# Performance work log

Hardware: AMD Instinct MI355X
Metric: run time of the kernel (lower is better)

## Reference

```python
import jax, jax.numpy as jnp
import numpy as np

B, T, C, H = 2, 2048, 1024, 16
Dh = C // H  # 64
EPS = 1e-5


def layer_norm(x, g, b):
    mu = jnp.mean(x, axis=-1, keepdims=True)
    var = jnp.mean(jnp.square(x - mu), axis=-1, keepdims=True)
    return (x - mu) * jax.lax.rsqrt(var + EPS) * g + b


def setup_inputs() -> dict:
    key = jax.random.key(0)
    ks = jax.random.split(key, 12)
    s = 0.02
    return {
        "x": jax.random.normal(ks[0], (B, T, C), dtype=jnp.float32),
        # per-head projections, stacked: (H, C, Dh), no bias (bias=False in source)
        "Wq": jax.random.normal(ks[1], (H, C, Dh), dtype=jnp.float32) * s,
        "Wk": jax.random.normal(ks[2], (H, C, Dh), dtype=jnp.float32) * s,
        "Wv": jax.random.normal(ks[3], (H, C, Dh), dtype=jnp.float32) * s,
        "Wo": jax.random.normal(ks[4], (H * Dh, C), dtype=jnp.float32) * s,
        "bo": jnp.zeros((C,), dtype=jnp.float32),
        "W1": jax.random.normal(ks[5], (C, 4 * C), dtype=jnp.float32) * s,
        "b1": jnp.zeros((4 * C,), dtype=jnp.float32),
        "W2": jax.random.normal(ks[6], (4 * C, C), dtype=jnp.float32) * s,
        "b2": jnp.zeros((C,), dtype=jnp.float32),
        "g1": jnp.ones((C,), dtype=jnp.float32),
        "be1": jnp.zeros((C,), dtype=jnp.float32),
        "g2": jnp.ones((C,), dtype=jnp.float32),
        "be2": jnp.zeros((C,), dtype=jnp.float32),
    }


def reference(x, Wq, Wk, Wv, Wo, bo, W1, b1, W2, b2, g1, be1, g2, be2):
    # --- self-attention sublayer ---
    h = layer_norm(x, g1, be1)                       # (B,T,C)
    q = jnp.einsum("btc,hcd->bhtd", h, Wq)
    k = jnp.einsum("btc,hcd->bhtd", h, Wk)
    v = jnp.einsum("btc,hcd->bhtd", h, Wv)
    # NOTE: source scales by C**-0.5 (head INPUT dim), not head_size**-0.5
    scores = jnp.einsum("bhqd,bhkd->bhqk", q, k) * (C ** -0.5)
    # encoder=True default => mask is all ones => no masking applied
    w = jax.nn.softmax(scores, axis=-1)              # (B,H,T,T)
    o = jnp.einsum("bhqk,bhkd->bhqd", w, v)          # (B,H,T,Dh)
    o = o.transpose(0, 2, 1, 3).reshape(B, T, H * Dh)  # concat heads
    attn = o @ Wo + bo                               # output projection
    x = x + attn
    # --- feed-forward sublayer ---
    h2 = layer_norm(x, g2, be2)
    ff = jax.nn.relu(h2 @ W1 + b1) @ W2 + b2
    return x + ff
```

## Files before the change

kernel.cpp:

```cpp
#include <hip/hip_runtime.h>
#include <hip/hip_bf16.h>

#define BT   4096
#define CD   1024
#define TD   2048
#define NH   16
#define DH   64
#define BB   2

typedef __attribute__((ext_vector_type(8))) short bf16x8;
typedef __attribute__((ext_vector_type(4))) short bf16x4;
typedef __attribute__((ext_vector_type(4))) float f32x4;
typedef __attribute__((ext_vector_type(2))) unsigned int u32x2;
typedef __attribute__((ext_vector_type(4))) unsigned int u32x4;

__device__ inline short f2bf(float f) {
    union { float fv; unsigned u; } x; x.fv = f;
    unsigned r = x.u + 0x7fffu + ((x.u >> 16) & 1u);
    return (short)(r >> 16);
}
__device__ inline float bf2f(short s) {
    union { unsigned u; float f; } x; x.u = ((unsigned)(unsigned short)s) << 16;
    return x.f;
}
__device__ inline unsigned pk2bf(float a, float b) {
    union { __hip_bfloat162 h; unsigned u; } cv;
    cv.h = __float22bfloat162_rn(float2{a, b});
    return cv.u;
}

#if __has_builtin(__builtin_amdgcn_exp2f)
#define EXP2(x) __builtin_amdgcn_exp2f(x)
#else
#define EXP2(x) exp2f(x)
#endif

__device__ inline void gload_lds16(const short* g, short* lds) {
    __builtin_amdgcn_global_load_lds(
        (const __attribute__((address_space(1))) void*)g,
        (__attribute__((address_space(3))) void*)lds, 16, 0, 0);
}

__launch_bounds__(256)
__global__ void ln_kernel(const float* __restrict__ x,
                          const float* __restrict__ g,
                          const float* __restrict__ be,
                          short* __restrict__ out) {
    __shared__ float red[2][4];
    const int row = blockIdx.x;
    const float* xr = x + (size_t)row * CD;
    float s = 0.f, ss = 0.f;
    for (int c = threadIdx.x; c < CD; c += 256) {
        float v = xr[c];
        s += v; ss += v * v;
    }
    #pragma unroll
    for (int off = 32; off > 0; off >>= 1) {
        s  += __shfl_down(s,  off, 64);
        ss += __shfl_down(ss, off, 64);
    }
    int wid = threadIdx.x >> 6, lane = threadIdx.x & 63;
    if (lane == 0) { red[0][wid] = s; red[1][wid] = ss; }
    __syncthreads();
    float sum   = red[0][0] + red[0][1] + red[0][2] + red[0][3];
    float sumsq = red[1][0] + red[1][1] + red[1][2] + red[1][3];
    float mu   = sum * (1.f / CD);
    float var  = sumsq * (1.f / CD) - mu * mu;
    float rstd = rsqrtf(var + 1e-5f);
    short* orow = out + (size_t)row * CD;
    for (int c = threadIdx.x; c < CD; c += 256) {
        float v = xr[c];
        orow[c] = f2bf((v - mu) * rstd * g[c] + be[c]);
    }
}

__launch_bounds__(256)
__global__ void prep_weights(const float* __restrict__ Wq, const float* __restrict__ Wk,
                             const float* __restrict__ Wv, const float* __restrict__ Wo,
                             const float* __restrict__ W1, const float* __restrict__ W2,
                             short* __restrict__ wqt, short* __restrict__ wot,
                             short* __restrict__ w1t, short* __restrict__ w2t) {
    __shared__ float tt[64][65];
    const int id = blockIdx.x;
    const float* in; short* out; int R, Cc, r0, c0;
    if (id < 768) {
        int which = id >> 8, rem = id & 255, hh = rem >> 4, ry = rem & 15;
        in  = (which == 0 ? Wq : which == 1 ? Wk : Wv) + (size_t)hh * CD * DH;
        out = wqt + (size_t)which * CD * CD + (size_t)hh * DH * CD;
        R = CD; Cc = DH; r0 = ry * 64; c0 = 0;
    } else if (id < 1024) {
        int t = id - 768;  in = Wo; out = wot; R = CD;     Cc = CD;     r0 = (t >> 4) * 64; c0 = (t & 15) * 64;
    } else if (id < 2048) {
        int t = id - 1024; in = W1; out = w1t; R = CD;     Cc = 4 * CD; r0 = (t >> 6) * 64; c0 = (t & 63) * 64;
    } else {
        int t = id - 2048; in = W2; out = w2t; R = 4 * CD; Cc = CD;     r0 = (t >> 4) * 64; c0 = (t & 15) * 64;
    }
    const int tid = threadIdx.x;
    #pragma unroll
    for (int i = 0; i < 16; ++i) {
        int e = i * 256 + tid;
        tt[e >> 6][e & 63] = in[(size_t)(r0 + (e >> 6)) * Cc + c0 + (e & 63)];
    }
    __syncthreads();
    #pragma unroll
    for (int i = 0; i < 16; ++i) {
        int e = i * 256 + tid;
        out[(size_t)(c0 + (e >> 6)) * R + r0 + (e & 63)] = f2bf(tt[e & 63][e >> 6]);
    }
}

__launch_bounds__(256)
__global__ void vtrans(const short* __restrict__ vin, short* __restrict__ vout) {
    __shared__ short t[64 * 65];
    const int tid = threadIdx.x;
    const int bh = blockIdx.y;
    const int t0 = blockIdx.x * 64;
    const int b = bh >> 4, h = bh & 15;
    const short* src = vin + (size_t)b * TD * CD + (size_t)h * DH;
    short* dst = vout + (size_t)bh * DH * TD;
    #pragma unroll
    for (int i = 0; i < 16; ++i) {
        int e = i * 256 + tid;
        t[(e >> 6) * 65 + (e & 63)] = src[(size_t)(t0 + (e >> 6)) * CD + (e & 63)];
    }
    __syncthreads();
    #pragma unroll
    for (int i = 0; i < 16; ++i) {
        int e = i * 256 + tid;
        int d = e >> 6, tt = e & 63;
        dst[(size_t)d * TD + t0 + tt] = t[tt * 65 + d];
    }
}

template <int MODE, int TN, int GR>
__launch_bounds__(GR * 256)
__global__ void gemm_mfma(const short* __restrict__ A,
                          const short* __restrict__ Bt,
                          const float* __restrict__ bias,
                          const float* __restrict__ resid,
                          float* __restrict__ outf,
                          short* __restrict__ outb,
                          int N, int K) {
    __shared__ __align__(16) short smem[GR * 3 * (128 + TN) * 32];
    const int tid = threadIdx.x;
    const int kgrp = (GR == 2) ? (tid >> 8) : 0;
    const int tid256 = tid & 255;
    const int w4 = tid256 >> 6, lane = tid & 63;
    const int quad = lane >> 4, l16 = lane & 15;
    const int wr = w4 >> 1, wc = w4 & 1;
    const int li = blockIdx.y * gridDim.x + blockIdx.x;
    const int m0 = ((li & 7) * 4 + ((li >> 3) & 3)) * 128;
    const int n0 = (li >> 5) * TN;
    const int NT = TN / 32;
    const int kbase = kgrp * (K / GR);

    short* grpBase = smem + (size_t)kgrp * 3 * (128 + TN) * 32;
#define AS(bi) (grpBase + (bi) * (128 + TN) * 32)
#define BS(bi) (AS(bi) + 128 * 32)

    f32x4 acc[4][NT] = {};

    auto STAGE = [&](int kt, int bi) {
        const int k0 = kbase + kt * 32;
        short* as = AS(bi);
        short* bs = BS(bi);
        #pragma unroll
        for (int i = 0; i < 2; ++i) {
            int s = i * 256 + tid256;
            int row = s >> 2, kc = (s & 3) ^ ((row >> 1) & 3);
            gload_lds16(A + (size_t)(m0 + row) * K + k0 + kc * 8,
                        &as[(i * 256 + w4 * 64) * 8]);
        }
        #pragma unroll
        for (int i = 0; i < TN / 64; ++i) {
            int s = i * 256 + tid256;
            int row = s >> 2, kc = (s & 3) ^ ((row >> 1) & 3);
            gload_lds16(Bt + (size_t)(n0 + row) * K + k0 + kc * 8,
                        &bs[(i * 256 + w4 * 64) * 8]);
        }
    };

    auto COMPUTE = [&](int bi) {
        const int xo = (quad ^ ((l16 >> 1) & 3)) * 8;
        const short* as = AS(bi);
        const short* bs = BS(bi);
        bf16x8 a[4], b[NT];
        #pragma unroll
        for (int mt = 0; mt < 4; ++mt)
            a[mt] = *(const bf16x8*)&as[(wr * 64 + mt * 16 + l16) * 32 + xo];
        #pragma unroll
        for (int nt = 0; nt < NT; ++nt)
            b[nt] = *(const bf16x8*)&bs[(wc * (TN / 2) + nt * 16 + l16) * 32 + xo];
        #pragma unroll
        for (int mt = 0; mt < 4; ++mt)
            #pragma unroll
            for (int nt = 0; nt < NT; ++nt)
                acc[mt][nt] = __builtin_amdgcn_mfma_f32_16x16x32_bf16(a[mt], b[nt], acc[mt][nt], 0, 0, 0);
    };

    const int nk = (K / GR) >> 5;
    STAGE(0, 0);
    STAGE(1, 1);
    int bi = 0;
    for (int t = 0; t < nk - 1; ++t) {
        asm volatile("s_waitcnt vmcnt(4)" ::: "memory");
        __builtin_amdgcn_s_barrier();
        asm volatile("" ::: "memory");
        int bn = bi + 2 >= 3 ? bi - 1 : bi + 2;
        if (t + 2 < nk) STAGE(t + 2, bn);
        COMPUTE(bi);
        bi = bi + 1 >= 3 ? 0 : bi + 1;
    }
    asm volatile("s_waitcnt vmcnt(0)" ::: "memory");
    __builtin_amdgcn_s_barrier();
    asm volatile("" ::: "memory");
    COMPUTE(bi);

    if (GR == 2) {
        float* red = (float*)smem;
        __syncthreads();
        if (kgrp == 1) {
            #pragma unroll
            for (int mt = 0; mt < 4; ++mt)
                #pragma unroll
                for (int nt = 0; nt < NT; ++nt)
                    *(f32x4*)&red[((mt * NT + nt) * 256 + w4 * 64 + lane) * 4] = acc[mt][nt];
        }
        __syncthreads();
        if (kgrp == 1) return;
        #pragma unroll
        for (int mt = 0; mt < 4; ++mt)
            #pragma unroll
            for (int nt = 0; nt < NT; ++nt) {
                f32x4 p = *(const f32x4*)&red[((mt * NT + nt) * 256 + w4 * 64 + lane) * 4];
                acc[mt][nt] += p;
            }
    }

    const float qsc = (MODE == 5 && n0 < CD) ? 0.03125f * 1.44269504f : 1.0f;
    short* ob5 = (MODE == 5) ? outb + (size_t)(n0 >> 10) * BT * CD : nullptr;

    #pragma unroll
    for (int mt = 0; mt < 4; ++mt)
        #pragma unroll
        for (int nt = 0; nt < NT; ++nt)
            #pragma unroll
            for (int reg = 0; reg < 4; ++reg) {
                int row = m0 + wr * 64 + mt * 16 + quad * 4 + reg;
                int col = n0 + wc * (TN / 2) + nt * 16 + l16;
                float v = acc[mt][nt][reg];
                if (MODE == 1) { v += bias[col] + resid[(size_t)row * N + col];
                                 outf[(size_t)row * N + col] = v; }
                if (MODE == 2) { v = fmaxf(v + bias[col], 0.f);
                                 outb[(size_t)row * N + col] = f2bf(v); }
                if (MODE == 5) { ob5[(size_t)row * CD + (col & 1023)] = f2bf(v * qsc); }
            }
#undef AS
#undef BS
}

#define BQ   128
#define BK   64
#define STR  68

__launch_bounds__(256)
__global__ void attn_mfma(const short* __restrict__ q,
                          const short* __restrict__ k,
                          const short* __restrict__ vt,
                          short* __restrict__ opart,
                          float* __restrict__ lpart) {
    __shared__ short Ks[2][BK * STR];
    __shared__ short Vt[2][DH * STR];

    const int tid  = threadIdx.x;
    const int w = tid >> 6, lane = tid & 63;
    const int quad = lane >> 4, l16 = lane & 15;
    const int h = blockIdx.y;
    const int b = blockIdx.z >> 1, split = blockIdx.z & 1;
    const int q0 = blockIdx.x * BQ;
    const size_t base  = (size_t)b * TD * CD + (size_t)h * DH;
    const size_t vbase = (size_t)(b * NH + h) * DH * TD;

    bf16x8 qf[2][2];
    #pragma unroll
    for (int rt = 0; rt < 2; ++rt) {
        const short* qp = q + base + (size_t)(q0 + w * 32 + rt * 16 + l16) * CD;
        qf[rt][0] = *(const bf16x8*)&qp[quad * 8];
        qf[rt][1] = *(const bf16x8*)&qp[32 + quad * 8];
    }

    float l_p[2] = {};
    f32x4 O[2][4] = {};

    const int kbeg = split * (TD / 2);
    const int NTI = (TD / 2) / BK;

    const int r8 = tid >> 3, c8 = (tid & 7) * 8;
    const int s32 = ((r8 & 4) << 2) + ((r8 >> 3) << 2) + (r8 & 3);
    const short* kg = k + base + c8;
    const short* vg = vt + vbase + (size_t)r8 * TD + c8;

#define ISSUE_T(t, K0, K1, V0, V1) do {                                   \
        const size_t ko_ = (size_t)(kbeg + (t) * BK);                     \
        K0 = *(const bf16x8*)&kg[(ko_ + r8) * CD];                        \
        K1 = *(const bf16x8*)&kg[(ko_ + r8 + 32) * CD];                   \
        V0 = *(const bf16x8*)&vg[ko_];                                    \
        V1 = *(const bf16x8*)&vg[(size_t)32 * TD + ko_];                  \
    } while (0)

#define WRITE_T(buf, K0, K1, V0, V1) do {                                 \
        *(bf16x8*)&Ks[buf][s32 * STR + c8] = K0;                          \
        *(bf16x8*)&Ks[buf][(s32 + 32) * STR + c8] = K1;                   \
        *(bf16x8*)&Vt[buf][r8 * STR + c8] = V0;                           \
        *(bf16x8*)&Vt[buf][(r8 + 32) * STR + c8] = V1;                    \
    } while (0)

#define COMPUTE_T(buf) do {                                               \
        __builtin_amdgcn_s_setprio(1);                                    \
        _Pragma("unroll")                                                 \
        for (int sp = 0; sp < 2; ++sp) {                                  \
            bf16x8 kbe0 = *(const bf16x8*)&Ks[buf][(sp * 32 + l16) * STR + quad * 8];      \
            bf16x8 kbe1 = *(const bf16x8*)&Ks[buf][(sp * 32 + l16) * STR + 32 + quad * 8]; \
            bf16x8 kbo0 = *(const bf16x8*)&Ks[buf][(sp * 32 + 16 + l16) * STR + quad * 8]; \
            bf16x8 kbo1 = *(const bf16x8*)&Ks[buf][(sp * 32 + 16 + l16) * STR + 32 + quad * 8]; \
            bf16x8 pa8[2];                                                \
            _Pragma("unroll")                                             \
            for (int rt = 0; rt < 2; ++rt) {                              \
                f32x4 ae = (f32x4){0.f, 0.f, 0.f, 0.f};                   \
                f32x4 ao = (f32x4){0.f, 0.f, 0.f, 0.f};                   \
                ae = __builtin_amdgcn_mfma_f32_16x16x32_bf16(kbe0, qf[rt][0], ae, 0, 0, 0); \
                ae = __builtin_amdgcn_mfma_f32_16x16x32_bf16(kbe1, qf[rt][1], ae, 0, 0, 0); \
                ao = __builtin_amdgcn_mfma_f32_16x16x32_bf16(kbo0, qf[rt][0], ao, 0, 0, 0); \
                ao = __builtin_amdgcn_mfma_f32_16x16x32_bf16(kbo1, qf[rt][1], ao, 0, 0, 0); \
                float pe0 = EXP2(ae[0]), pe1 = EXP2(ae[1]);               \
                float pe2 = EXP2(ae[2]), pe3 = EXP2(ae[3]);               \
                float po0 = EXP2(ao[0]), po1 = EXP2(ao[1]);               \
                float po2 = EXP2(ao[2]), po3 = EXP2(ao[3]);               \
                l_p[rt] += ((pe0 + pe1) + (pe2 + pe3)) + ((po0 + po1) + (po2 + po3)); \
                union { u32x4 u; bf16x8 s; } cv_;                         \
                cv_.u = (u32x4){pk2bf(pe0, pe1), pk2bf(pe2, pe3),         \
                                pk2bf(po0, po1), pk2bf(po2, po3)};        \
                pa8[rt] = cv_.s;                                          \
            }                                                             \
            _Pragma("unroll")                                             \
            for (int dt = 0; dt < 4; ++dt) {                              \
                bf16x8 vb = *(const bf16x8*)&Vt[buf][(dt * 16 + l16) * STR + sp * 32 + quad * 8]; \
                O[0][dt] = __builtin_amdgcn_mfma_f32_16x16x32_bf16(pa8[0], vb, O[0][dt], 0, 0, 0); \
                O[1][dt] = __builtin_amdgcn_mfma_f32_16x16x32_bf16(pa8[1], vb, O[1][dt], 0, 0, 0); \
            }                                                             \
        }                                                                 \
        __builtin_amdgcn_s_setprio(0);                                    \
    } while (0)

    bf16x8 kA0, kA1, vA0, vA1;
    bf16x8 kB0, kB1, vB0, vB1;

    ISSUE_T(0, kA0, kA1, vA0, vA1);
    WRITE_T(0, kA0, kA1, vA0, vA1);
    ISSUE_T(1, kA0, kA1, vA0, vA1);
    __syncthreads();

    for (int it = 0; it < NTI; it += 2) {
        if (it + 2 < NTI) ISSUE_T(it + 2, kB0, kB1, vB0, vB1);
        COMPUTE_T(0);
        WRITE_T(1, kA0, kA1, vA0, vA1);
        __syncthreads();
        if (it + 3 < NTI) ISSUE_T(it + 3, kA0, kA1, vA0, vA1);
        COMPUTE_T(1);
        if (it + 2 < NTI) WRITE_T(0, kB0, kB1, vB0, vB1);
        __syncthreads();
    }
#undef ISSUE_T
#undef WRITE_T
#undef COMPUTE_T

    short* osp = opart + (size_t)split * BT * CD;
    float* lsp = lpart + (size_t)split * BB * NH * TD + (size_t)(b * NH + h) * TD;
    #pragma unroll
    for (int rt = 0; rt < 2; ++rt) {
        float l = l_p[rt];
        l += __shfl_xor(l, 16, 64);
        l += __shfl_xor(l, 32, 64);
        if (lane < 16) lsp[q0 + w * 32 + rt * 16 + lane] = l;
        #pragma unroll
        for (int reg = 0; reg < 4; ++reg) {
            int row = q0 + w * 32 + rt * 16 + quad * 4 + reg;
            short* op = osp + base + (size_t)row * CD;
            #pragma unroll
            for (int dt = 0; dt < 4; ++dt)
                op[dt * 16 + l16] = f2bf(O[rt][dt][reg]);
        }
    }
}

__launch_bounds__(256)
__global__ void attn_combine(const short* __restrict__ opart,
                             const float* __restrict__ lpart,
                             short* __restrict__ ob) {
    const size_t idx = ((size_t)blockIdx.x * 256 + threadIdx.x) * 8;
    const int row = (int)(idx >> 10);
    const int col = (int)(idx & 1023);
    const int b = row >> 11, qq = row & (TD - 1), hh = col >> 6;
    const size_t lbase = (size_t)(b * NH + hh) * TD + qq;
    const float l0 = lpart[lbase];
    const float l1 = lpart[(size_t)BB * NH * TD + lbase];
    const float inv = 1.f / (l0 + l1);
    bf16x8 a = *(const bf16x8*)&opart[idx];
    bf16x8 c = *(const bf16x8*)&opart[(size_t)BT * CD + idx];
    bf16x8 r;
    #pragma unroll
    for (int j = 0; j < 8; ++j)
        r[j] = f2bf((bf2f(a[j]) + bf2f(c[j])) * inv);
    *(bf16x8*)&ob[idx] = r;
}

extern "C" void kernel_launch(void* const* d_in, const int* in_sizes, int n_in,
                              void* d_out, int out_size, void* d_ws, size_t ws_size,
                              hipStream_t stream) {
    const float* x   = (const float*)d_in[0];
    const float* Wq  = (const float*)d_in[1];
    const float* Wk  = (const float*)d_in[2];
    const float* Wv  = (const float*)d_in[3];
    const float* Wo  = (const float*)d_in[4];
    const float* bo  = (const float*)d_in[5];
    const float* W1  = (const float*)d_in[6];
    const float* b1  = (const float*)d_in[7];
    const float* W2  = (const float*)d_in[8];
    const float* b2  = (const float*)d_in[9];
    const float* g1  = (const float*)d_in[10];
    const float* be1 = (const float*)d_in[11];
    const float* g2  = (const float*)d_in[12];
    const float* be2 = (const float*)d_in[13];
    float* out = (float*)d_out;

    const size_t SZ = (size_t)BT * CD;
    float* ws  = (float*)d_ws;
    short* qbf = (short*)ws;
    short* kbf = qbf + SZ;
    short* vbf = qbf + 2 * SZ;
    float* lpart = ws + SZ + SZ / 2;
    short* opart = (short*)(ws + 2 * SZ);
    float* x1  = ws + 2 * SZ;
    short* h   = (short*)(ws + 3 * SZ);
    short* ob  = (short*)(ws + 3 * SZ + SZ / 2);
    short* wqt = (short*)(ws + 4 * SZ);
    short* wot = wqt + 3 * CD * CD;
    short* w1t = (short*)(ws + 4 * SZ + SZ / 2);
    short* w2t = (short*)(ws + 5 * SZ);
    short* vtg = (short*)(ws + 5 * SZ + SZ / 2);
    short* ff1 = (short*)ws;

    ln_kernel<<<BT, 256, 0, stream>>>(x, g1, be1, h);

    prep_weights<<<3072, 256, 0, stream>>>(Wq, Wk, Wv, Wo, W1, W2, wqt, wot, w1t, w2t);

    gemm_mfma<5, 128, 1><<<dim3(24, 32), 256, 0, stream>>>(h, wqt, nullptr, nullptr, nullptr, qbf, 3 * CD, CD);

    vtrans<<<dim3(TD / 64, 2 * NH), 256, 0, stream>>>(vbf, vtg);

    attn_mfma<<<dim3(TD / BQ, NH, BB * 2), 256, 0, stream>>>(qbf, kbf, vtg, opart, lpart);

    attn_combine<<<dim3((int)(SZ / (256 * 8))), 256, 0, stream>>>(opart, lpart, ob);

    gemm_mfma<1, 128, 2><<<dim3(8, 32), 512, 0, stream>>>(ob, wot, bo, x, x1, nullptr, CD, CD);

    ln_kernel<<<BT, 256, 0, stream>>>(x1, g2, be2, h);

    gemm_mfma<2, 128, 1><<<dim3(32, 32), 256, 0, stream>>>(h, w1t, b1, nullptr, nullptr, ff1, 4 * CD, CD);

    gemm_mfma<1, 128, 2><<<dim3(8, 32), 512, 0, stream>>>(ff1, w2t, b2, x1, out, nullptr, CD, 4 * CD);
}
```

Baseline: 324.0 us.

## Compute softmax row sums via MFMA with ones and vectorize LN/prep loads

```diff
diff --git a/kernel.cpp b/kernel.cpp
--- a/kernel.cpp
+++ b/kernel.cpp
@@ -48,12 +48,11 @@
                           short* __restrict__ out) {
     __shared__ float red[2][4];
     const int row = blockIdx.x;
+    const int c4 = threadIdx.x * 4;
     const float* xr = x + (size_t)row * CD;
-    float s = 0.f, ss = 0.f;
-    for (int c = threadIdx.x; c < CD; c += 256) {
-        float v = xr[c];
-        s += v; ss += v * v;
-    }
+    float4 v = *(const float4*)&xr[c4];
+    float s  = (v.x + v.y) + (v.z + v.w);
+    float ss = (v.x * v.x + v.y * v.y) + (v.z * v.z + v.w * v.w);
     #pragma unroll
     for (int off = 32; off > 0; off >>= 1) {
         s  += __shfl_down(s,  off, 64);
@@ -67,11 +66,14 @@
     float mu   = sum * (1.f / CD);
     float var  = sumsq * (1.f / CD) - mu * mu;
     float rstd = rsqrtf(var + 1e-5f);
-    short* orow = out + (size_t)row * CD;
-    for (int c = threadIdx.x; c < CD; c += 256) {
-        float v = xr[c];
-        orow[c] = f2bf((v - mu) * rstd * g[c] + be[c]);
-    }
+    float4 gv = *(const float4*)&g[c4];
+    float4 bv = *(const float4*)&be[c4];
+    bf16x4 o;
+    o[0] = f2bf((v.x - mu) * rstd * gv.x + bv.x);
+    o[1] = f2bf((v.y - mu) * rstd * gv.y + bv.y);
+    o[2] = f2bf((v.z - mu) * rstd * gv.z + bv.z);
+    o[3] = f2bf((v.w - mu) * rstd * gv.w + bv.w);
+    *(bf16x4*)&out[(size_t)row * CD + c4] = o;
 }
 
 __launch_bounds__(256)
@@ -97,9 +99,14 @@
     }
     const int tid = threadIdx.x;
     #pragma unroll
-    for (int i = 0; i < 16; ++i) {
-        int e = i * 256 + tid;
-        tt[e >> 6][e & 63] = in[(size_t)(r0 + (e >> 6)) * Cc + c0 + (e & 63)];
+    for (int i = 0; i < 4; ++i) {
+        int f = i * 256 + tid;
+        int r = f >> 4, cc = (f & 15) * 4;
+        float4 vv = *(const float4*)&in[(size_t)(r0 + r) * Cc + c0 + cc];
+        tt[r][cc]     = vv.x;
+        tt[r][cc + 1] = vv.y;
+        tt[r][cc + 2] = vv.z;
+        tt[r][cc + 3] = vv.w;
     }
     __syncthreads();
     #pragma unroll
@@ -289,7 +296,9 @@
         qf[rt][1] = *(const bf16x8*)&qp[32 + quad * 8];
     }
 
-    float l_p[2] = {};
+    const bf16x8 ones = {(short)0x3F80, (short)0x3F80, (short)0x3F80, (short)0x3F80,
+                         (short)0x3F80, (short)0x3F80, (short)0x3F80, (short)0x3F80};
+    f32x4 O_l[2] = {};
     f32x4 O[2][4] = {};
 
     const int kbeg = split * (TD / 2);
@@ -336,7 +345,6 @@
                 float pe2 = EXP2(ae[2]), pe3 = EXP2(ae[3]);               \
                 float po0 = EXP2(ao[0]), po1 = EXP2(ao[1]);               \
                 float po2 = EXP2(ao[2]), po3 = EXP2(ao[3]);               \
-                l_p[rt] += ((pe0 + pe1) + (pe2 + pe3)) + ((po0 + po1) + (po2 + po3)); \
                 union { u32x4 u; bf16x8 s; } cv_;                         \
                 cv_.u = (u32x4){pk2bf(pe0, pe1), pk2bf(pe2, pe3),         \
                                 pk2bf(po0, po1), pk2bf(po2, po3)};        \
@@ -348,6 +356,8 @@
                 O[0][dt] = __builtin_amdgcn_mfma_f32_16x16x32_bf16(pa8[0], vb, O[0][dt], 0, 0, 0); \
                 O[1][dt] = __builtin_amdgcn_mfma_f32_16x16x32_bf16(pa8[1], vb, O[1][dt], 0, 0, 0); \
             }                                                             \
+            O_l[0] = __builtin_amdgcn_mfma_f32_16x16x32_bf16(pa8[0], ones, O_l[0], 0, 0, 0); \
+            O_l[1] = __builtin_amdgcn_mfma_f32_16x16x32_bf16(pa8[1], ones, O_l[1], 0, 0, 0); \
         }                                                                 \
         __builtin_amdgcn_s_setprio(0);                                    \
     } while (0)
@@ -378,10 +388,8 @@
     float* lsp = lpart + (size_t)split * BB * NH * TD + (size_t)(b * NH + h) * TD;
     #pragma unroll
     for (int rt = 0; rt < 2; ++rt) {
-        float l = l_p[rt];
-        l += __shfl_xor(l, 16, 64);
-        l += __shfl_xor(l, 32, 64);
-        if (lane < 16) lsp[q0 + w * 32 + rt * 16 + lane] = l;
+        if (l16 == 0)
+            *(f32x4*)&lsp[q0 + w * 32 + rt * 16 + quad * 4] = O_l[rt];
         #pragma unroll
         for (int reg = 0; reg < 4; ++reg) {
             int row = q0 + w * 32 + rt * 16 + quad * 4 + reg;
```

After: 317.9 us. No clear change (-1.9%).
